# Performance work log

Hardware: AMD Instinct MI355X
Metric: run time of the kernel (lower is better)

## Reference

```python
import jax, jax.numpy as jnp
import numpy as np

N = 200_000      # active voxels
INC = 64
OUTC = 96
GRID = 128
EPS = 1e-5


def _build_neighbor_maps():
    """Precompute gather/scatter index maps for the 26 off-center hypercube
    offsets (the 4th kernel dim has size 1, so offsets live in 3D)."""
    rng = np.random.default_rng(0)
    G = GRID ** 3
    lin = rng.choice(G, size=N, replace=False).astype(np.int64)
    z = lin % GRID
    y = (lin // GRID) % GRID
    x = lin // (GRID * GRID)
    lookup = np.full(G, -1, np.int64)
    lookup[lin] = np.arange(N)
    offsets = [(dx, dy, dz) for dx in (-1, 0, 1) for dy in (-1, 0, 1)
               for dz in (-1, 0, 1) if (dx, dy, dz) != (0, 0, 0)]
    pin, pout = [], []
    for dx, dy, dz in offsets:
        nx, ny, nz = x + dx, y + dy, z + dz
        valid = (nx >= 0) & (nx < GRID) & (ny >= 0) & (ny < GRID) & (nz >= 0) & (nz < GRID)
        nlin = (nx * GRID + ny) * GRID + nz
        nb = np.where(valid, lookup[np.clip(nlin, 0, G - 1)], -1)
        m = nb >= 0
        pin.append(np.arange(N)[m])
        pout.append(nb[m])
    pmax = max(len(p) for p in pin)
    in_idx = np.zeros((26, pmax), np.int64)          # pad gathers row 0 (harmless)
    out_idx = np.full((26, pmax), N, np.int64)       # pad scatters to sink row N
    for k, (pi, po) in enumerate(zip(pin, pout)):
        in_idx[k, : len(pi)] = pi
        out_idx[k, : len(po)] = po
    return in_idx, out_idx


def setup_inputs() -> dict:
    in_idx, out_idx = _build_neighbor_maps()
    key = jax.random.key(0)
    k1, k2, k3 = jax.random.split(key, 3)
    std = 1.0 / np.sqrt(INC * 27)
    feats = jax.random.normal(k1, (N, INC), jnp.float32)
    W_center = jax.random.normal(k2, (INC, OUTC), jnp.float32) * std
    W_off = jax.random.normal(k3, (26, INC, OUTC), jnp.float32) * std
    gamma = jnp.ones((OUTC,), jnp.float32)   # bn.weight init to 1.0
    beta = jnp.zeros((OUTC,), jnp.float32)   # bn.bias init to 0.0
    return {"feats": feats, "W_center": W_center, "W_off": W_off,
            "gamma": gamma, "beta": beta,
            "in_idx": jnp.asarray(in_idx), "out_idx": jnp.asarray(out_idx)}


def reference(feats, W_center, W_off, gamma, beta, in_idx, out_idx):
    # --- sparse conv-transpose: gather -> GEMM -> scatter-add ---
    out = feats @ W_center                                   # center offset: identity map, [N, outc]
    gathered = feats[in_idx]                                 # [26, P, inc]
    contrib = jnp.einsum('kpc,kcd->kpd', gathered, W_off)    # [26, P, outc]
    out = jnp.concatenate([out, jnp.zeros((1, OUTC), out.dtype)], axis=0)  # sink row
    out = out.at[out_idx.reshape(-1)].add(contrib.reshape(-1, OUTC))[:N]
    # --- BatchNorm (training-mode batch stats) + ReLU ---
    mean = out.mean(axis=0)
    var = out.var(axis=0)
    y = (out - mean) * jax.lax.rsqrt(var + EPS) * gamma + beta
    return jax.nn.relu(y)
```

## Files before the change

kernel.cpp:

```cpp
#include <hip/hip_runtime.h>


#define N_VOX   200000
#define INC     64
#define OUTC    96
#define NOFF    26
#define MROWS   192
#define NBLK    1042
#define NPAD    200192
#define EPSV    1e-5f

using bf16x8 = __attribute__((ext_vector_type(8))) short;
using f32x4  = __attribute__((ext_vector_type(4))) float;

__device__ inline unsigned short f2bf(float x) {
    union { float f; unsigned u; } v; v.f = x;
    unsigned r = (v.u + 0x7FFFu + ((v.u >> 16) & 1u)) >> 16;
    return (unsigned short)r;
}

__device__ __forceinline__ void gload_lds16(const void* g, void* l) {
    __builtin_amdgcn_global_load_lds(
        (const __attribute__((address_space(1))) void*)g,
        (__attribute__((address_space(3))) void*)l, 16, 0, 0);
}

__global__ void prep_kernel(const float* __restrict__ feats,
                            const float* __restrict__ Wc,
                            const float* __restrict__ Woff,
                            const int* __restrict__ in_idx,
                            const int* __restrict__ out_idx,
                            int P, int fill_blocks,
                            unsigned short* __restrict__ featsb,
                            unsigned short* __restrict__ Wb,
                            int* __restrict__ srcmap) {
    const int FCVT_BLOCKS = (N_VOX * INC / 8 + 255) / 256;
    int b = blockIdx.x;
    int t = threadIdx.x;
    if (b < FCVT_BLOCKS) {
        int i = b * 256 + t;
        if (i < N_VOX * INC / 8) {
            const float4* src = (const float4*)feats + (size_t)i * 2;
            float4 f0 = src[0], f1 = src[1];
            bf16x8 v;
            v[0] = (short)f2bf(f0.x); v[1] = (short)f2bf(f0.y);
            v[2] = (short)f2bf(f0.z); v[3] = (short)f2bf(f0.w);
            v[4] = (short)f2bf(f1.x); v[5] = (short)f2bf(f1.y);
            v[6] = (short)f2bf(f1.z); v[7] = (short)f2bf(f1.w);
            *(bf16x8*)(featsb + (size_t)i * 8) = v;
        }
        return;
    }
    b -= FCVT_BLOCKS;
    if (b < fill_blocks) {
        int idx = b * 256 + t;
        if (idx < NOFF * P) {
            int dst = out_idx[idx];
            if (dst < N_VOX) {
                int k = idx / P;
                srcmap[(size_t)k * NPAD + dst] = in_idx[idx];
            }
        }
        return;
    }
    b -= fill_blocks;
    {
        int g = b * 256 + t;
        if (g >= 27 * 2 * 6 * 64) return;
        int lane = g & 63;
        int gg   = g >> 6;
        int ct   = gg % 6;
        int s    = (gg / 6) % 2;
        int m    = gg / 12;
        const float* W = (m == 26) ? Wc : (Woff + (size_t)m * INC * OUTC);
        int k0 = s * 32 + (lane >> 4) * 8;
        int c  = ct * 16 + (lane & 15);
        bf16x8 v;
        #pragma unroll
        for (int e = 0; e < 8; ++e)
            v[e] = (short)f2bf(W[(size_t)(k0 + e) * OUTC + c]);
        *(bf16x8*)(Wb + (size_t)g * 8) = v;
    }
}

template<int STAGE_BF16>
__global__ __launch_bounds__(256, 3)
void conv_mfma_kernel(const unsigned short* __restrict__ featsb,
                      const unsigned short* __restrict__ Wb,
                      const int* __restrict__ srcmap,
                      float* __restrict__ outf,
                      unsigned short* __restrict__ stg,
                      float* __restrict__ pstats) {
    __shared__ __align__(16) unsigned short Wlds[4][6144];

    const int t     = threadIdx.x;
    const int wid   = t >> 6;
    const int lane  = t & 63;
    const int blk   = blockIdx.x;
    const int rbase = blk * MROWS + wid * 48;
    const int row16 = lane & 15;
    const int kgrp  = lane >> 4;

    f32x4  acc[3][6] = {};
    bf16x8 aC[3][2], aN[3][2];

    #pragma unroll
    for (int i = 0; i < 3; ++i)
        gload_lds16(Wb + (size_t)26 * 6144 + (size_t)(t + 256 * i) * 8,
                    &Wlds[0][(t + 256 * i) * 8]);
    #pragma unroll
    for (int i = 0; i < 3; ++i)
        gload_lds16(Wb + (size_t)(t + 256 * i) * 8,
                    &Wlds[1][(t + 256 * i) * 8]);

    int sm_next = (lane < 48) ? srcmap[rbase + lane] : -1;

    bool has_cur = true;
    #pragma unroll
    for (int rt = 0; rt < 3; ++rt) {
        int row = rbase + rt * 16 + row16;
        int src = row < N_VOX ? row : N_VOX;
        const unsigned short* fr = featsb + (size_t)src * INC + kgrp * 8;
        aC[rt][0] = *(const bf16x8*)fr;
        aC[rt][1] = *(const bf16x8*)(fr + 32);
    }
    __syncthreads();

    for (int idx = 0; idx < 27; ++idx) {
        int sm_next2 = -1;
        if (idx <= 24 && lane < 48)
            sm_next2 = srcmap[(size_t)(idx + 1) * NPAD + rbase + lane];

        bool has_next = false;
        if (idx <= 25) {
            bool any = false;
            #pragma unroll
            for (int rt = 0; rt < 3; ++rt) {
                int src = __shfl(sm_next, rt * 16 + row16);
                bf16x8 g0 = {}, g1 = {};
                if (src >= 0) {
                    const unsigned short* fr = featsb + (size_t)src * INC + kgrp * 8;
                    g0 = *(const bf16x8*)fr;
                    g1 = *(const bf16x8*)(fr + 32);
                    any = true;
                }
                aN[rt][0] = g0; aN[rt][1] = g1;
            }
            has_next = __ballot(any) != 0ull;
        }
        if (idx <= 24) {
            #pragma unroll
            for (int i = 0; i < 3; ++i)
                gload_lds16(Wb + (size_t)(idx + 1) * 6144 + (size_t)(t + 256 * i) * 8,
                            &Wlds[(idx + 2) & 3][(t + 256 * i) * 8]);
        }

        if (has_cur) {
            const unsigned short* WL = Wlds[idx & 3];
            #pragma unroll
            for (int ct = 0; ct < 6; ++ct) {
                bf16x8 b0 = *(const bf16x8*)&WL[(size_t)ct * 512 + lane * 8];
                bf16x8 b1 = *(const bf16x8*)&WL[(size_t)(6 + ct) * 512 + lane * 8];
                #pragma unroll
                for (int rt = 0; rt < 3; ++rt) {
                    acc[rt][ct] = __builtin_amdgcn_mfma_f32_16x16x32_bf16(aC[rt][0], b0, acc[rt][ct], 0, 0, 0);
                    acc[rt][ct] = __builtin_amdgcn_mfma_f32_16x16x32_bf16(aC[rt][1], b1, acc[rt][ct], 0, 0, 0);
                }
            }
        }

        if (idx & 1) __syncthreads();

        #pragma unroll
        for (int rt = 0; rt < 3; ++rt) { aC[rt][0] = aN[rt][0]; aC[rt][1] = aN[rt][1]; }
        sm_next = sm_next2;
        has_cur = has_next;
    }

    float s6[6], q6[6];
    #pragma unroll
    for (int ct = 0; ct < 6; ++ct) {
        float s = 0.f, q = 0.f;
        #pragma unroll
        for (int rt = 0; rt < 3; ++rt) {
            f32x4 a = acc[rt][ct];
            s += a[0] + a[1] + a[2] + a[3];
            q += a[0]*a[0] + a[1]*a[1] + a[2]*a[2] + a[3]*a[3];
        }
        s += __shfl_xor(s, 16); q += __shfl_xor(q, 16);
        s += __shfl_xor(s, 32); q += __shfl_xor(q, 32);
        s6[ct] = s; q6[ct] = q;
    }
    float* sred = (float*)Wlds;
    if (lane < 16) {
        #pragma unroll
        for (int ct = 0; ct < 6; ++ct) {
            sred[wid * 96 + ct * 16 + lane]       = s6[ct];
            sred[384 + wid * 96 + ct * 16 + lane] = q6[ct];
        }
    }
    __syncthreads();
    if (t < 96) {
        float s = sred[t] + sred[96 + t] + sred[192 + t] + sred[288 + t];
        pstats[(size_t)t * NBLK + blk] = s;
    } else if (t < 192) {
        int c = t - 96;
        float q = sred[384 + c] + sred[480 + c] + sred[576 + c] + sred[672 + c];
        pstats[(size_t)(96 + c) * NBLK + blk] = q;
    }

    #pragma unroll
    for (int rt = 0; rt < 3; ++rt) {
        #pragma unroll
        for (int ct = 0; ct < 6; ++ct) {
            #pragma unroll
            for (int j = 0; j < 4; ++j) {
                int row = rbase + rt * 16 + kgrp * 4 + j;
                if (row < N_VOX) {
                    if (STAGE_BF16)
                        stg[(size_t)row * OUTC + ct * 16 + row16] = f2bf(acc[rt][ct][j]);
                    else
                        outf[(size_t)row * OUTC + ct * 16 + row16] = acc[rt][ct][j];
                }
            }
        }
    }
}

__global__ void stats_reduce_kernel(const float* __restrict__ pstats,
                                    const float* __restrict__ gamma,
                                    const float* __restrict__ beta,
                                    float* __restrict__ scsh) {
    int c = blockIdx.x;
    int t = threadIdx.x;
    float s = 0.f, q = 0.f;
    for (int i = t; i < NBLK; i += 256) {
        s += pstats[(size_t)c * NBLK + i];
        q += pstats[(size_t)(96 + c) * NBLK + i];
    }
    #pragma unroll
    for (int d = 1; d < 64; d <<= 1) {
        s += __shfl_xor(s, d);
        q += __shfl_xor(q, d);
    }
    __shared__ float rs[4], rq[4];
    if ((t & 63) == 0) { rs[t >> 6] = s; rq[t >> 6] = q; }
    __syncthreads();
    if (t == 0) {
        s = rs[0] + rs[1] + rs[2] + rs[3];
        q = rq[0] + rq[1] + rq[2] + rq[3];
        float inv_n = 1.0f / (float)N_VOX;
        float mean = s * inv_n;
        float var  = q * inv_n - mean * mean;
        float sc   = gamma[c] * rsqrtf(var + EPSV);
        scsh[c]      = sc;
        scsh[96 + c] = beta[c] - mean * sc;
    }
}

__global__ void apply_bn_bf16_kernel(const unsigned short* __restrict__ stg,
                                     float* __restrict__ out,
                                     const float* __restrict__ scsh) {
    __shared__ float sc[OUTC], sh[OUTC];
    int t = threadIdx.x;
    if (t < OUTC) { sc[t] = scsh[t]; sh[t] = scsh[96 + t]; }
    __syncthreads();
    const int total8 = N_VOX * OUTC / 8;
    for (int i = blockIdx.x * blockDim.x + t; i < total8; i += gridDim.x * blockDim.x) {
        bf16x8 v = *(const bf16x8*)(stg + (size_t)i * 8);
        int c = (i % 12) * 8;
        float o[8];
        #pragma unroll
        for (int j = 0; j < 8; ++j) {
            union { unsigned u; float f; } w; w.u = (unsigned)(unsigned short)v[j] << 16;
            o[j] = fmaxf(fmaf(w.f, sc[c + j], sh[c + j]), 0.f);
        }
        float4* dst = (float4*)(out + (size_t)i * 8);
        dst[0] = make_float4(o[0], o[1], o[2], o[3]);
        dst[1] = make_float4(o[4], o[5], o[6], o[7]);
    }
}

__global__ void apply_bn_fp32_kernel(float* __restrict__ out,
                                     const float* __restrict__ scsh) {
    __shared__ float sc[OUTC], sh[OUTC];
    int t = threadIdx.x;
    if (t < OUTC) { sc[t] = scsh[t]; sh[t] = scsh[96 + t]; }
    __syncthreads();
    const int total4 = N_VOX * OUTC / 4;
    for (int i = blockIdx.x * blockDim.x + t; i < total4; i += gridDim.x * blockDim.x) {
        float4 v = ((float4*)out)[i];
        int c = (i * 4) % OUTC;
        v.x = fmaxf(fmaf(v.x, sc[c    ], sh[c    ]), 0.f);
        v.y = fmaxf(fmaf(v.y, sc[c + 1], sh[c + 1]), 0.f);
        v.z = fmaxf(fmaf(v.z, sc[c + 2], sh[c + 2]), 0.f);
        v.w = fmaxf(fmaf(v.w, sc[c + 3], sh[c + 3]), 0.f);
        ((float4*)out)[i] = v;
    }
}

extern "C" void kernel_launch(void* const* d_in, const int* in_sizes, int n_in,
                              void* d_out, int out_size, void* d_ws, size_t ws_size,
                              hipStream_t stream) {
    const float* feats   = (const float*)d_in[0];
    const float* Wc      = (const float*)d_in[1];
    const float* Woff    = (const float*)d_in[2];
    const float* gamma   = (const float*)d_in[3];
    const float* beta    = (const float*)d_in[4];
    const int*   in_idx  = (const int*)d_in[5];
    const int*   out_idx = (const int*)d_in[6];
    const int P = in_sizes[5] / NOFF;

    char* w = (char*)d_ws;
    int* srcmap = (int*)w;                   w += (size_t)NOFF * NPAD * 4;
    unsigned short* Wb = (unsigned short*)w; w += (size_t)27 * 6144 * 2;
    float* pstats = (float*)w;               w += (size_t)192 * NBLK * 4;
    float* scsh = (float*)w;                 w += 256 * 4;
    unsigned short* featsb = (unsigned short*)w;
    w += (size_t)(N_VOX + 1) * INC * 2;
    unsigned short* stg = (unsigned short*)w;
    size_t need_stg = (size_t)(w - (char*)d_ws) + (size_t)N_VOX * OUTC * 2;
    bool use_stg = (ws_size >= need_stg);

    hipMemsetAsync(srcmap, 0xFF, (size_t)NOFF * NPAD * 4, stream);
    hipMemsetAsync(featsb + (size_t)N_VOX * INC, 0, INC * 2, stream);

    const int FCVT_BLOCKS = (N_VOX * INC / 8 + 255) / 256;
    const int fill_blocks = (NOFF * P + 255) / 256;
    const int WPREP_BLOCKS = (27 * 2 * 6 * 64 + 255) / 256;
    prep_kernel<<<FCVT_BLOCKS + fill_blocks + WPREP_BLOCKS, 256, 0, stream>>>(
        feats, Wc, Woff, in_idx, out_idx, P, fill_blocks, featsb, Wb, srcmap);

    float* out = (float*)d_out;
    if (use_stg) {
        conv_mfma_kernel<1><<<NBLK, 256, 0, stream>>>(featsb, Wb, srcmap, out, stg, pstats);
        stats_reduce_kernel<<<96, 256, 0, stream>>>(pstats, gamma, beta, scsh);
        apply_bn_bf16_kernel<<<2048, 256, 0, stream>>>(stg, out, scsh);
    } else {
        conv_mfma_kernel<0><<<NBLK, 256, 0, stream>>>(featsb, Wb, srcmap, out, stg, pstats);
        stats_reduce_kernel<<<96, 256, 0, stream>>>(pstats, gamma, beta, scsh);
        apply_bn_fp32_kernel<<<2048, 256, 0, stream>>>(out, scsh);
    }
}
```

Baseline: 114.5 us.

## Simplify conv pipeline, shrink LDS for higher occupancy, fuse BN stats via atomics

Result: slower. 134.9 us (+17.8%).

```diff
diff --git a/kernel.cpp b/kernel.cpp
--- a/kernel.cpp
+++ b/kernel.cpp
@@ -84,14 +84,14 @@
 }
 
 template<int STAGE_BF16>
-__global__ __launch_bounds__(256, 3)
+__global__ __launch_bounds__(256, 4)
 void conv_mfma_kernel(const unsigned short* __restrict__ featsb,
                       const unsigned short* __restrict__ Wb,
                       const int* __restrict__ srcmap,
                       float* __restrict__ outf,
                       unsigned short* __restrict__ stg,
-                      float* __restrict__ pstats) {
-    __shared__ __align__(16) unsigned short Wlds[4][6144];
+                      float* __restrict__ stats) {
+    __shared__ __align__(16) unsigned short Wlds[2][6144];
 
     const int t     = threadIdx.x;
     const int wid   = t >> 6;
@@ -101,66 +101,66 @@
     const int row16 = lane & 15;
     const int kgrp  = lane >> 4;
 
-    f32x4  acc[3][6] = {};
-    bf16x8 aC[3][2], aN[3][2];
+    f32x4 acc[3][6] = {};
+    int smA[3], smB[3];
 
     #pragma unroll
     for (int i = 0; i < 3; ++i)
-        gload_lds16(Wb + (size_t)26 * 6144 + (size_t)(t + 256 * i) * 8,
+        gload_lds16(Wb + 26 * 6144 + (unsigned)(t + 256 * i) * 8,
                     &Wlds[0][(t + 256 * i) * 8]);
     #pragma unroll
-    for (int i = 0; i < 3; ++i)
-        gload_lds16(Wb + (size_t)(t + 256 * i) * 8,
-                    &Wlds[1][(t + 256 * i) * 8]);
-
-    int sm_next = (lane < 48) ? srcmap[rbase + lane] : -1;
-
-    bool has_cur = true;
-    #pragma unroll
     for (int rt = 0; rt < 3; ++rt) {
-        int row = rbase + rt * 16 + row16;
-        int src = row < N_VOX ? row : N_VOX;
-        const unsigned short* fr = featsb + (size_t)src * INC + kgrp * 8;
-        aC[rt][0] = *(const bf16x8*)fr;
-        aC[rt][1] = *(const bf16x8*)(fr + 32);
+        smA[rt] = -1;
+        smB[rt] = srcmap[(unsigned)(rbase + rt * 16 + row16)];
     }
     __syncthreads();
 
     for (int idx = 0; idx < 27; ++idx) {
-        int sm_next2 = -1;
-        if (idx <= 24 && lane < 48)
-            sm_next2 = srcmap[(size_t)(idx + 1) * NPAD + rbase + lane];
-
-        bool has_next = false;
-        if (idx <= 25) {
-            bool any = false;
+        const int buf = idx & 1;
+
+        bf16x8 aC[3][2];
+        if (idx == 0) {
             #pragma unroll
             for (int rt = 0; rt < 3; ++rt) {
-                int src = __shfl(sm_next, rt * 16 + row16);
+                int row = rbase + rt * 16 + row16;
+                unsigned src = (row < N_VOX ? row : N_VOX) * INC;
+                const unsigned short* fr = featsb + src + kgrp * 8;
+                aC[rt][0] = *(const bf16x8*)fr;
+                aC[rt][1] = *(const bf16x8*)(fr + 32);
+            }
+        } else {
+            #pragma unroll
+            for (int rt = 0; rt < 3; ++rt) {
+                int s = smA[rt];
                 bf16x8 g0 = {}, g1 = {};
-                if (src >= 0) {
-                    const unsigned short* fr = featsb + (size_t)src * INC + kgrp * 8;
+                if (s >= 0) {
+                    const unsigned short* fr = featsb + (unsigned)s * INC + kgrp * 8;
                     g0 = *(const bf16x8*)fr;
                     g1 = *(const bf16x8*)(fr + 32);
-                    any = true;
                 }
-                aN[rt][0] = g0; aN[rt][1] = g1;
-            }
-            has_next = __ballot(any) != 0ull;
-        }
+                aC[rt][0] = g0; aC[rt][1] = g1;
+            }
+        }
+
+        if (idx <= 25) {
+            #pragma unroll
+            for (int i = 0; i < 3; ++i)
+                gload_lds16(Wb + (unsigned)idx * 6144 + (unsigned)(t + 256 * i) * 8,
+                            &Wlds[buf ^ 1][(t + 256 * i) * 8]);
+        }
+        int smN[3];
         if (idx <= 24) {
             #pragma unroll
-            for (int i = 0; i < 3; ++i)
-                gload_lds16(Wb + (size_t)(idx + 1) * 6144 + (size_t)(t + 256 * i) * 8,
-                            &Wlds[(idx + 2) & 3][(t + 256 * i) * 8]);
-        }
-
-        if (has_cur) {
-            const unsigned short* WL = Wlds[idx & 3];
+            for (int rt = 0; rt < 3; ++rt)
+                smN[rt] = srcmap[(unsigned)(idx + 1) * NPAD + rbase + rt * 16 + row16];
+        }
+
+        {
+            const unsigned short* WL = Wlds[buf];
             #pragma unroll
             for (int ct = 0; ct < 6; ++ct) {
-                bf16x8 b0 = *(const bf16x8*)&WL[(size_t)ct * 512 + lane * 8];
-                bf16x8 b1 = *(const bf16x8*)&WL[(size_t)(6 + ct) * 512 + lane * 8];
+                bf16x8 b0 = *(const bf16x8*)&WL[ct * 512 + lane * 8];
+                bf16x8 b1 = *(const bf16x8*)&WL[(6 + ct) * 512 + lane * 8];
                 #pragma unroll
                 for (int rt = 0; rt < 3; ++rt) {
                     acc[rt][ct] = __builtin_amdgcn_mfma_f32_16x16x32_bf16(aC[rt][0], b0, acc[rt][ct], 0, 0, 0);
@@ -168,13 +168,13 @@
                 }
             }
         }
-
-        if (idx & 1) __syncthreads();
-
-        #pragma unroll
-        for (int rt = 0; rt < 3; ++rt) { aC[rt][0] = aN[rt][0]; aC[rt][1] = aN[rt][1]; }
-        sm_next = sm_next2;
-        has_cur = has_next;
+        __syncthreads();
+
+        #pragma unroll
+        for (int rt = 0; rt < 3; ++rt) {
+            smA[rt] = smB[rt];
+            smB[rt] = (idx <= 24) ? smN[rt] : -1;
+        }
     }
 
     float s6[6], q6[6];
@@ -202,11 +202,11 @@
     __syncthreads();
     if (t < 96) {
         float s = sred[t] + sred[96 + t] + sred[192 + t] + sred[288 + t];
-        pstats[(size_t)t * NBLK + blk] = s;
+        atomicAdd(&stats[t], s);
     } else if (t < 192) {
         int c = t - 96;
         float q = sred[384 + c] + sred[480 + c] + sred[576 + c] + sred[672 + c];
-        pstats[(size_t)(96 + c) * NBLK + blk] = q;
+        atomicAdd(&stats[96 + c], q);
     }
 
     #pragma unroll
@@ -227,43 +227,22 @@
     }
 }
 
-__global__ void stats_reduce_kernel(const float* __restrict__ pstats,
-                                    const float* __restrict__ gamma,
-                                    const float* __restrict__ beta,
-                                    float* __restrict__ scsh) {
-    int c = blockIdx.x;
-    int t = threadIdx.x;
-    float s = 0.f, q = 0.f;
-    for (int i = t; i < NBLK; i += 256) {
-        s += pstats[(size_t)c * NBLK + i];
-        q += pstats[(size_t)(96 + c) * NBLK + i];
-    }
-    #pragma unroll
-    for (int d = 1; d < 64; d <<= 1) {
-        s += __shfl_xor(s, d);
-        q += __shfl_xor(q, d);
-    }
-    __shared__ float rs[4], rq[4];
-    if ((t & 63) == 0) { rs[t >> 6] = s; rq[t >> 6] = q; }
-    __syncthreads();
-    if (t == 0) {
-        s = rs[0] + rs[1] + rs[2] + rs[3];
-        q = rq[0] + rq[1] + rq[2] + rq[3];
-        float inv_n = 1.0f / (float)N_VOX;
-        float mean = s * inv_n;
-        float var  = q * inv_n - mean * mean;
-        float sc   = gamma[c] * rsqrtf(var + EPSV);
-        scsh[c]      = sc;
-        scsh[96 + c] = beta[c] - mean * sc;
-    }
-}
-
-__global__ void apply_bn_bf16_kernel(const unsigned short* __restrict__ stg,
-                                     float* __restrict__ out,
-                                     const float* __restrict__ scsh) {
+__global__ __launch_bounds__(256, 8)
+void apply_bn_bf16_kernel(const unsigned short* __restrict__ stg,
+                          float* __restrict__ out,
+                          const float* __restrict__ stats,
+                          const float* __restrict__ gamma,
+                          const float* __restrict__ beta) {
     __shared__ float sc[OUTC], sh[OUTC];
     int t = threadIdx.x;
-    if (t < OUTC) { sc[t] = scsh[t]; sh[t] = scsh[96 + t]; }
+    if (t < OUTC) {
+        float inv_n = 1.0f / (float)N_VOX;
+        float mean = stats[t] * inv_n;
+        float var  = stats[96 + t] * inv_n - mean * mean;
+        float s    = gamma[t] * rsqrtf(var + EPSV);
+        sc[t] = s;
+        sh[t] = beta[t] - mean * s;
+    }
     __syncthreads();
     const int total8 = N_VOX * OUTC / 8;
     for (int i = blockIdx.x * blockDim.x + t; i < total8; i += gridDim.x * blockDim.x) {
@@ -281,11 +260,21 @@
     }
 }
 
-__global__ void apply_bn_fp32_kernel(float* __restrict__ out,
-                                     const float* __restrict__ scsh) {
+__global__ __launch_bounds__(256, 8)
+void apply_bn_fp32_kernel(float* __restrict__ out,
+                          const float* __restrict__ stats,
+                          const float* __restrict__ gamma,
+                          const float* __restrict__ beta) {
     __shared__ float sc[OUTC], sh[OUTC];
     int t = threadIdx.x;
-    if (t < OUTC) { sc[t] = scsh[t]; sh[t] = scsh[96 + t]; }
+    if (t < OUTC) {
+        float inv_n = 1.0f / (float)N_VOX;
+        float mean = stats[t] * inv_n;
+        float var  = stats[96 + t] * inv_n - mean * mean;
+        float s    = gamma[t] * rsqrtf(var + EPSV);
+        sc[t] = s;
+        sh[t] = beta[t] - mean * s;
+    }
     __syncthreads();
     const int total4 = N_VOX * OUTC / 4;
     for (int i = blockIdx.x * blockDim.x + t; i < total4; i += gridDim.x * blockDim.x) {
@@ -314,8 +303,7 @@
     char* w = (char*)d_ws;
     int* srcmap = (int*)w;                   w += (size_t)NOFF * NPAD * 4;
     unsigned short* Wb = (unsigned short*)w; w += (size_t)27 * 6144 * 2;
-    float* pstats = (float*)w;               w += (size_t)192 * NBLK * 4;
-    float* scsh = (float*)w;                 w += 256 * 4;
+    float* stats = (float*)w;                w += 256 * 4;
     unsigned short* featsb = (unsigned short*)w;
     w += (size_t)(N_VOX + 1) * INC * 2;
     unsigned short* stg = (unsigned short*)w;
@@ -323,6 +311,7 @@
     bool use_stg = (ws_size >= need_stg);
 
     hipMemsetAsync(srcmap, 0xFF, (size_t)NOFF * NPAD * 4, stream);
+    hipMemsetAsync(stats, 0, 192 * 4, stream);
     hipMemsetAsync(featsb + (size_t)N_VOX * INC, 0, INC * 2, stream);
 
     const int FCVT_BLOCKS = (N_VOX * INC / 8 + 255) / 256;
@@ -333,12 +322,10 @@
 
     float* out = (float*)d_out;
     if (use_stg) {
-        conv_mfma_kernel<1><<<NBLK, 256, 0, stream>>>(featsb, Wb, srcmap, out, stg, pstats);
-        stats_reduce_kernel<<<96, 256, 0, stream>>>(pstats, gamma, beta, scsh);
-        apply_bn_bf16_kernel<<<2048, 256, 0, stream>>>(stg, out, scsh);
+        conv_mfma_kernel<1><<<NBLK, 256, 0, stream>>>(featsb, Wb, srcmap, out, stg, stats);
+        apply_bn_bf16_kernel<<<2048, 256, 0, stream>>>(stg, out, stats, gamma, beta);
     } else {
-        conv_mfma_kernel<0><<<NBLK, 256, 0, stream>>>(featsb, Wb, srcmap, out, stg, pstats);
-        stats_reduce_kernel<<<96, 256, 0, stream>>>(pstats, gamma, beta, scsh);
-        apply_bn_fp32_kernel<<<2048, 256, 0, stream>>>(out, scsh);
-    }
-}
+        conv_mfma_kernel<0><<<NBLK, 256, 0, stream>>>(featsb, Wb, srcmap, out, stg, stats);
+        apply_bn_fp32_kernel<<<2048, 256, 0, stream>>>(out, stats, gamma, beta);
+    }
+}
```
